# Kernel optimization log

Measured on AMD Instinct MI355X. Metric: run time of the kernel, lower is better.

Reference implementation:

```python
import jax, jax.numpy as jnp
import numpy as np
from jax import lax

HEADS = 8
AGENT = 49            # agent_num
POOL = 7              # int(sqrt(agent_num))
DOWN_H, DOWN_W = 7, 7  # downstream_agent_shape
DIM = 256
WIN = 56              # sqrt(num_patches)


def _resize(x, oh, ow):
    # torch F.interpolate(mode='bilinear', align_corners=False) equivalent for upsample/identity
    return jax.image.resize(x, x.shape[:-2] + (oh, ow), method='bilinear', antialias=False)


def _bias_pipeline(bias, H, W):
    # bias: (heads, AGENT, h0, w0) -> (heads, H*W, DOWN_H*DOWN_W)
    h = bias.shape[0]
    pb = _resize(bias, H, W)                                     # (h, 49, H, W)
    pb = pb.reshape(h, POOL, POOL, H * W).transpose(0, 3, 1, 2)  # (h, HW, 7, 7)
    pb = _resize(pb, DOWN_H, DOWN_W)                             # (h, HW, 7, 7)
    return pb.reshape(h, H * W, DOWN_H * DOWN_W)


def setup_inputs() -> dict:
    key = jax.random.key(0)
    ks = jax.random.split(key, 16)
    b, H, W = 16, WIN, WIN
    n, c, h = H * W, DIM, HEADS
    s = 0.02
    f32 = jnp.float32
    return {
        "x": jax.random.normal(ks[0], (b, n, c), f32),
        "H": H,
        "W": W,
        "Wq": jax.random.normal(ks[1], (c, c), f32) * c ** -0.5,
        "Wkv": jax.random.normal(ks[2], (2 * c, c), f32) * c ** -0.5,
        "Wproj": jax.random.normal(ks[3], (c, c), f32) * c ** -0.5,
        "bproj": jnp.zeros((c,), f32),
        "dwc_w": jax.random.normal(ks[4], (c, 1, 3, 3), f32) * 0.1,
        "dwc_b": jnp.zeros((c,), f32),
        "an_bias": jax.random.normal(ks[5], (h, AGENT, 7, 7), f32) * s,
        "na_bias": jax.random.normal(ks[6], (h, AGENT, 7, 7), f32) * s,
        "ah_bias": jax.random.normal(ks[7], (1, h, AGENT, WIN, 1), f32) * s,
        "aw_bias": jax.random.normal(ks[8], (1, h, AGENT, 1, WIN), f32) * s,
        "ha_bias": jax.random.normal(ks[9], (1, h, WIN, 1, AGENT), f32) * s,
        "wa_bias": jax.random.normal(ks[10], (1, h, 1, WIN, AGENT), f32) * s,
    }


def reference(x, H, W, Wq, Wkv, Wproj, bproj, dwc_w, dwc_b,
              an_bias, na_bias, ah_bias, aw_bias, ha_bias, wa_bias):
    b, n, c = x.shape
    h = HEADS
    hd = c // h
    T = n // 2
    scale = hd ** -0.5
    dan = DOWN_H * DOWN_W

    q_lin = x @ Wq.T                       # (b,n,c)
    kv = x @ Wkv.T                         # (b,n,2c)
    k_lin, v_lin = kv[..., :c], kv[..., c:]

    # adaptive avg pool of q to (7,7) agent grid (H, W divisible by 7)
    qg = q_lin.reshape(b, DOWN_H, H // DOWN_H, DOWN_W, W // DOWN_W, c).mean(axis=(2, 4))
    agent = qg.reshape(b, dan, h, hd).transpose(0, 2, 1, 3)   # (b,h,49,hd)

    q = q_lin.reshape(b, n, h, hd).transpose(0, 2, 1, 3)      # (b,h,n,hd)
    k = k_lin.reshape(b, n, h, hd).transpose(0, 2, 1, 3)
    v = v_lin.reshape(b, n, h, hd).transpose(0, 2, 1, 3)

    # agent -> kv attention biases
    pb1 = _bias_pipeline(an_bias, H, W).transpose(0, 2, 1)    # (h,49,HW)
    pb2 = _bias_pipeline((ah_bias + aw_bias)[0], H, W).transpose(0, 2, 1)
    position_bias = (pb1 + pb2)[None]                         # (1,h,49,HW)

    agent_attn = jax.nn.softmax(
        jnp.einsum('bhad,bhnd->bhan', agent * scale, k) + position_bias, axis=-1)
    agent_v = jnp.einsum('bhan,bhnd->bhad', agent_attn, v)    # (b,h,49,hd)

    # query -> agent attention biases
    ab1 = _bias_pipeline(na_bias, H, W)                       # (h,HW,49)
    ab2 = _bias_pipeline((ha_bias + wa_bias)[0].transpose(0, 3, 1, 2), H, W)
    agent_bias = (ab1 + ab2)[None]                            # (1,h,HW,49)

    # top-T query selection, then bilinear upsample of scores back to n rows
    token_w = jax.nn.softmax(q.mean(axis=-1), axis=-1)        # (b,h,n)
    _, top_idx = lax.top_k(token_w, T)                        # (b,h,T)
    q_top = jnp.take_along_axis(q, top_idx[..., None], axis=2)  # (b,h,T,hd)
    q2 = jnp.einsum('bhtd,bhad->bhta', q_top, agent)          # (b,h,T,49)
    q2 = _resize(q2, n, dan) * scale                          # (b,h,n,49)

    q_attn = jax.nn.softmax(q2 + agent_bias, axis=-1)
    out = jnp.einsum('bhna,bhad->bhnd', q_attn, agent_v)
    out = out.transpose(0, 2, 1, 3).reshape(b, n, c)

    # depthwise conv branch on v
    v_img = v.transpose(0, 2, 1, 3).reshape(b, H, W, c).transpose(0, 3, 1, 2)  # (b,c,H,W)
    dw = lax.conv_general_dilated(v_img, dwc_w, (1, 1), ((1, 1), (1, 1)),
                                  feature_group_count=c)
    dw = dw + dwc_b[None, :, None, None]
    out = out + dw.transpose(0, 2, 3, 1).reshape(b, n, c)
    return out @ Wproj.T + bproj
```

## Files before the change

### kernel.cpp

```cpp
#include <hip/hip_runtime.h>
#include <stdint.h>

typedef _Float16 f16;
typedef _Float16 half8 __attribute__((ext_vector_type(8)));
typedef float f32x4 __attribute__((ext_vector_type(4)));

#define NBATCH 16
#define NTOK 3136
#define NTOT 50176
#define NH 8
#define NA 49
#define NAP 64
#define TTOP 1568
#define SCALE 0.17677669529663687f
#define FPARTS 4

__device__ __forceinline__ f32x4 mfma16(half8 a, half8 b, f32x4 c) {
  return __builtin_amdgcn_mfma_f32_16x16x32_f16(a, b, c, 0, 0, 0);
}

__device__ __forceinline__ void gload16(const void* g, void* l) {
  __builtin_amdgcn_global_load_lds(
      (const __attribute__((address_space(1))) void*)g,
      (__attribute__((address_space(3))) void*)l, 16, 0, 0);
}

__global__ __launch_bounds__(256) void k_prep_w(const float* Wq, const float* Wkv, const float* Wproj,
                                                f16* wqkv, f16* wproj) {
  int total1 = 768 * 256;
  int total = total1 + 256 * 256;
  for (int i = blockIdx.x * 256 + threadIdx.x; i < total; i += gridDim.x * 256) {
    if (i < total1) {
      int j = i >> 8, k = i & 255;
      float v = (j < 256) ? Wq[j * 256 + k] : Wkv[(j - 256) * 256 + k];
      wqkv[i] = (f16)v;
    } else {
      int i2 = i - total1;
      wproj[i2] = (f16)Wproj[i2];
    }
  }
}

__global__ __launch_bounds__(256) void k_cvt_x(const float* x, f16* xh, long total) {
  long i = (long)blockIdx.x * blockDim.x + threadIdx.x;
  long stride = (long)gridDim.x * blockDim.x;
  for (long e = i * 8; e < total; e += stride * 8) {
    float4 v0 = *(const float4*)(x + e);
    float4 v1 = *(const float4*)(x + e + 4);
    half8 o = {(f16)v0.x, (f16)v0.y, (f16)v0.z, (f16)v0.w,
               (f16)v1.x, (f16)v1.y, (f16)v1.z, (f16)v1.w};
    *(half8*)(xh + e) = o;
  }
}

__global__ __launch_bounds__(256) void k_bias(const float* an_b, const float* na_b,
                                              const float* ah_b, const float* aw_b,
                                              const float* ha_b, const float* wa_b,
                                              float* pos_bias, float* agent_bias) {
  int n = blockIdx.x * 256 + threadIdx.x;
  int h = blockIdx.y;
  if (n >= NTOK) return;
  int y = n / 56, x = n - y * 56;
  float py = (y + 0.5f) * 0.125f - 0.5f;
  float px = (x + 0.5f) * 0.125f - 0.5f;
  int iy0 = (int)floorf(py); float fy = py - (float)iy0;
  int ix0 = (int)floorf(px); float fx = px - (float)ix0;
  int y0 = max(iy0, 0), y1 = min(iy0 + 1, 6);
  int x0 = max(ix0, 0), x1 = min(ix0 + 1, 6);
  float w00 = (1.f - fy) * (1.f - fx), w01 = (1.f - fy) * fx;
  float w10 = fy * (1.f - fx), w11 = fy * fx;
  for (int a = 0; a < NA; ++a) {
    const float* pa = an_b + (h * NA + a) * 49;
    float up_an = w00 * pa[y0 * 7 + x0] + w01 * pa[y0 * 7 + x1] +
                  w10 * pa[y1 * 7 + x0] + w11 * pa[y1 * 7 + x1];
    const float* pn = na_b + (h * NA + a) * 49;
    float up_na = w00 * pn[y0 * 7 + x0] + w01 * pn[y0 * 7 + x1] +
                  w10 * pn[y1 * 7 + x0] + w11 * pn[y1 * 7 + x1];
    float pb = up_an + ah_b[(h * NA + a) * 56 + y] + aw_b[(h * NA + a) * 56 + x];
    pos_bias[((size_t)(h * NAP + a)) * NTOK + n] = pb;
    float ab = up_na + ha_b[(h * 56 + y) * NA + a] + wa_b[(h * 56 + x) * NA + a];
    agent_bias[((size_t)(h * NAP + a)) * NTOK + n] = ab;
  }
  for (int a = NA; a < NAP; ++a)
    pos_bias[((size_t)(h * NAP + a)) * NTOK + n] = 0.f;
}

template <bool PROJ>
__global__ __launch_bounds__(256) void k_gemm(const f16* __restrict__ A, const f16* __restrict__ Bw,
                                              f16* __restrict__ CH, float* __restrict__ Cf32,
                                              const float* __restrict__ bias, int N) {
  __shared__ __align__(16) char lds[16384];
  int per = gridDim.x >> 3;
  int wrk = (blockIdx.x & 7) * per + (blockIdx.x >> 3);
  int nNT = N >> 7;
  int mt = wrk / nNT, nt = wrk - mt * nNT;
  int m0 = mt * 128, n0 = nt * 128;
  int tid = threadIdx.x, w = tid >> 6, l = tid & 63, lr = l & 15, lg = l >> 4;
  int wm = w >> 1, wn = w & 1;
  f32x4 acc[4][4] = {};
  const char* Bb = (const char*)Bw + (size_t)n0 * 512;
  int rowA0 = 32 * w + (l >> 2);
  int rowA1 = rowA0 + 16;
  int koff = (l & 3) * 16;
  char* ldsA0 = lds + (2 * w) * 1024;
  char* ldsA1 = lds + (2 * w + 1) * 1024;
  char* ldsB0 = lds + 8192 + (2 * w) * 1024;
  char* ldsB1 = lds + 8192 + (2 * w + 1) * 1024;

  for (int k0 = 0; k0 < 256; k0 += 32) {
    if (PROJ) {
      const char* Ab = (const char*)A + ((size_t)(k0 >> 5) * NTOT + m0) * 64;
      gload16(Ab + (size_t)rowA0 * 64 + koff, ldsA0);
      gload16(Ab + (size_t)rowA1 * 64 + koff, ldsA1);
    } else {
      const char* Ab = (const char*)A + (size_t)m0 * 512 + k0 * 2;
      gload16(Ab + (size_t)rowA0 * 512 + koff, ldsA0);
      gload16(Ab + (size_t)rowA1 * 512 + koff, ldsA1);
    }
    gload16(Bb + (size_t)rowA0 * 512 + k0 * 2 + koff, ldsB0);
    gload16(Bb + (size_t)rowA1 * 512 + k0 * 2 + koff, ldsB1);
    __syncthreads();
    half8 af[4], bf[4];
#pragma unroll
    for (int m4 = 0; m4 < 4; ++m4) {
      int row = wm * 64 + m4 * 16 + lr;
      af[m4] = *(const half8*)(lds + row * 64 + lg * 16);
    }
#pragma unroll
    for (int n4 = 0; n4 < 4; ++n4) {
      int row = wn * 64 + n4 * 16 + lr;
      bf[n4] = *(const half8*)(lds + 8192 + row * 64 + lg * 16);
    }
#pragma unroll
    for (int m4 = 0; m4 < 4; ++m4)
#pragma unroll
      for (int n4 = 0; n4 < 4; ++n4)
        acc[m4][n4] = mfma16(af[m4], bf[n4], acc[m4][n4]);
    __syncthreads();
  }

  if (PROJ) {
#pragma unroll
    for (int n4 = 0; n4 < 4; ++n4) {
      int n = n0 + wn * 64 + n4 * 16 + lr;
#pragma unroll
      for (int m4 = 0; m4 < 4; ++m4)
#pragma unroll
        for (int r = 0; r < 4; ++r) {
          int m = m0 + wm * 64 + m4 * 16 + lg * 4 + r;
          Cf32[(size_t)m * N + n] = acc[m4][n4][r] + bias[n];
        }
    }
  } else {
    f16* cl = (f16*)lds;
    int rr = tid >> 2, c4 = tid & 3;
#pragma unroll
    for (int hm = 0; hm < 2; ++hm) {
      __syncthreads();
      if (wm == hm) {
#pragma unroll
        for (int m4 = 0; m4 < 4; ++m4)
#pragma unroll
          for (int n4 = 0; n4 < 4; ++n4)
#pragma unroll
            for (int r = 0; r < 4; ++r)
              cl[(m4 * 16 + lg * 4 + r) * 128 + wn * 64 + n4 * 16 + lr] = (f16)acc[m4][n4][r];
      }
      __syncthreads();
#pragma unroll
      for (int cc = 0; cc < 4; ++cc) {
        int pn = (n0 >> 5) + cc;
        half8 v = *(const half8*)(cl + rr * 128 + cc * 32 + c4 * 8);
        *(half8*)(CH + ((size_t)pn * NTOT + m0 + hm * 64 + rr) * 32 + c4 * 8) = v;
      }
    }
  }
}

__global__ __launch_bounds__(256) void k_pool_tw(const f16* qkvH, f16* agent, float* tw) {
  int bh = blockIdx.x, b = bh >> 3, h = bh & 7;
  int tid = threadIdx.x;
  const f16* qp0 = qkvH + ((size_t)h * NTOT + (size_t)b * NTOK) * 32;
  {
    int a = tid >> 2, c = tid & 3;
    float s8[8] = {};
    if (a < NA) {
      int dh = a / 7, dwi = a - dh * 7;
      for (int i = 0; i < 8; ++i)
#pragma unroll
        for (int j = 0; j < 8; ++j) {
          int tok = (dh * 8 + i) * 56 + dwi * 8 + j;
          half8 v = *(const half8*)(qp0 + (size_t)tok * 32 + c * 8);
#pragma unroll
          for (int e = 0; e < 8; ++e) s8[e] += (float)v[e];
        }
    }
    half8 o;
#pragma unroll
    for (int e = 0; e < 8; ++e) o[e] = (f16)(s8[e] * (SCALE / 64.f));
    *(half8*)(agent + (size_t)bh * NAP * 32 + a * 32 + c * 8) = o;
  }
  for (int n = tid; n < NTOK; n += 256) {
    const half8* qp = (const half8*)(qp0 + (size_t)n * 32);
    float sum = 0.f;
#pragma unroll
    for (int j = 0; j < 4; ++j) {
      half8 v = qp[j];
#pragma unroll
      for (int e = 0; e < 8; ++e) sum += (float)v[e];
    }
    tw[(size_t)bh * NTOK + n] = sum * (1.f / 32.f);
  }
}

template <int NE, int J>
__device__ __forceinline__ void stage_local(unsigned long long (&key)[NE], int kmask, int base) {
#pragma unroll
  for (int e = 0; e < NE; ++e) {
    if ((e & J) == 0) {
      bool desc = (((base + e) & kmask) == 0);
      unsigned long long a = key[e], c = key[e | J];
      if ((a < c) == desc) { key[e] = c; key[e | J] = a; }
    }
  }
}

__global__ __launch_bounds__(256, 1) void k_sort1(const float* tw, unsigned long long* keys64) {
  __shared__ unsigned long long lk[2048 + 128];
  int bh = blockIdx.x >> 1, half = blockIdx.x & 1;
  int tid = threadIdx.x;
  const float* p = tw + (size_t)bh * NTOK;
  int gbase = half * 2048 + tid * 8;
  unsigned long long key[8];
#pragma unroll
  for (int e = 0; e < 8; ++e) {
    int s = gbase + e;
    float v = (s < NTOK) ? p[s] : -1e30f;
    unsigned ub = __float_as_uint(v);
    ub = (ub & 0x80000000u) ? ~ub : (ub | 0x80000000u);
    unsigned low = (s < NTOK) ? ~(unsigned)s : 0u;
    key[e] = ((unsigned long long)ub << 32) | low;
  }
  stage_local<8, 1>(key, 2, gbase);
  stage_local<8, 2>(key, 4, gbase); stage_local<8, 1>(key, 4, gbase);
  stage_local<8, 4>(key, 8, gbase); stage_local<8, 2>(key, 8, gbase); stage_local<8, 1>(key, 8, gbase);
  for (int k = 16; k <= 2048; k <<= 1) {
    bool desc = ((gbase & k) == 0);
    for (int j = k >> 1; j >= 8; j >>= 1) {
      int m = j >> 3;
      bool takeMax = (((tid & m) == 0) == desc);
      unsigned long long pv[8];
      if (m <= 32) {
#pragma unroll
        for (int e = 0; e < 8; ++e) pv[e] = __shfl_xor(key[e], m, 64);
      } else {
        __syncthreads();
#pragma unroll
        for (int e = 0; e < 8; ++e) { int ix = tid * 8 + e; lk[ix + (ix >> 4)] = key[e]; }
        __syncthreads();
        int pb = (tid ^ m) * 8;
#pragma unroll
        for (int e = 0; e < 8; ++e) { int ix = pb + e; pv[e] = lk[ix + (ix >> 4)]; }
      }
#pragma unroll
      for (int e = 0; e < 8; ++e)
        key[e] = takeMax ? (key[e] > pv[e] ? key[e] : pv[e])
                         : (key[e] < pv[e] ? key[e] : pv[e]);
    }
    stage_local<8, 4>(key, k, gbase);
    stage_local<8, 2>(key, k, gbase);
    stage_local<8, 1>(key, k, gbase);
  }
  unsigned long long* op = keys64 + (size_t)bh * 4096 + gbase;
#pragma unroll
  for (int e = 0; e < 8; ++e) op[e] = key[e];
}

__global__ __launch_bounds__(256, 1) void k_sort2(const unsigned long long* keys64, int* topidx) {
  __shared__ unsigned long long lk[4096 + 256];
  int bh = blockIdx.x, tid = threadIdx.x;
  const unsigned long long* ip = keys64 + (size_t)bh * 4096 + (size_t)tid * 16;
  unsigned long long key[16];
#pragma unroll
  for (int e = 0; e < 16; ++e) key[e] = ip[e];
  int base = tid * 16;
  for (int j = 2048; j >= 16; j >>= 1) {
    int m = j >> 4;
    bool takeMax = ((tid & m) == 0);
    unsigned long long pv[16];
    if (m <= 32) {
#pragma unroll
      for (int e = 0; e < 16; ++e) pv[e] = __shfl_xor(key[e], m, 64);
    } else {
      __syncthreads();
#pragma unroll
      for (int e = 0; e < 16; ++e) { int ix = base + e; lk[ix + (ix >> 4)] = key[e]; }
      __syncthreads();
      int pb = (tid ^ m) * 16;
#pragma unroll
      for (int e = 0; e < 16; ++e) { int ix = pb + e; pv[e] = lk[ix + (ix >> 4)]; }
    }
#pragma unroll
    for (int e = 0; e < 16; ++e)
      key[e] = takeMax ? (key[e] > pv[e] ? key[e] : pv[e])
                       : (key[e] < pv[e] ? key[e] : pv[e]);
  }
  stage_local<16, 8>(key, 4096, base);
  stage_local<16, 4>(key, 4096, base);
  stage_local<16, 2>(key, 4096, base);
  stage_local<16, 1>(key, 4096, base);
  if (tid < TTOP / 16) {
    int* op = topidx + (size_t)bh * TTOP + base;
#pragma unroll
    for (int e = 0; e < 16; ++e) op[e] = (int)(~(unsigned)key[e]);
  }
}

__global__ __launch_bounds__(256) void k_vt(const f16* qkvH, f16* vt) {
  __shared__ __align__(16) f16 t[64][40];
  int bh = blockIdx.y, b = bh >> 3, h = bh & 7;
  int n0 = blockIdx.x * 64;
  int tid = threadIdx.x;
  const f16* vp = qkvH + ((size_t)(16 + h) * NTOT + (size_t)b * NTOK + n0) * 32;
  {
    int nl = tid >> 2, c = tid & 3;
    *(half8*)(&t[nl][c * 8]) = *(const half8*)(vp + (size_t)nl * 32 + c * 8);
  }
  __syncthreads();
  for (int s = tid; s < 64 * 32; s += 256) {
    int d = s >> 6, nl = s & 63;
    vt[((size_t)(bh * 32 + d)) * NTOK + n0 + nl] = t[nl][d];
  }
}

__global__ __launch_bounds__(256) void k_flash(const f16* qkvH, const f16* agent, const f16* vt,
                                               const float* pos_bias, float* opart, float* rspart) {
  __shared__ __align__(16) f16 pbuf[4][64][40];
  __shared__ float ored[64][33];
  __shared__ float rssum[64];
  int part = blockIdx.x, bh = blockIdx.y, b = bh >> 3, h = bh & 7;
  int tid = threadIdx.x, w = tid >> 6, l = tid & 63, lr = l & 15, lg = l >> 4;
  half8 afrag[4];
#pragma unroll
  for (int mt = 0; mt < 4; ++mt)
    afrag[mt] = *(const half8*)(agent + ((size_t)bh * 64 + mt * 16 + lr) * 32 + lg * 8);
  f32x4 o[4][2] = {};
  float rs[4][4] = {};
  const f16* kbase = qkvH + ((size_t)(8 + h) * NTOT + (size_t)b * NTOK) * 32;
  const f16* vtb = vt + (size_t)bh * 32 * NTOK;
  const float* pbb = pos_bias + (size_t)h * NAP * NTOK;
  f32x4 zero = {};
  for (int n0 = (part * 4 + w) * 32; n0 < NTOK; n0 += 512) {
#pragma unroll
    for (int t2 = 0; t2 < 2; ++t2) {
      int nc = n0 + t2 * 16;
      half8 kf = *(const half8*)(kbase + (size_t)(nc + lr) * 32 + lg * 8);
#pragma unroll
      for (int mt = 0; mt < 4; ++mt) {
        f32x4 s = mfma16(afrag[mt], kf, zero);
#pragma unroll
        for (int r = 0; r < 4; ++r) {
          int a = mt * 16 + lg * 4 + r;
          float pv = __expf(s[r] + pbb[(size_t)a * NTOK + nc + lr]);
          rs[mt][r] += pv;
          pbuf[w][a][t2 * 16 + lr] = (f16)pv;
        }
      }
    }
    half8 pf[4];
#pragma unroll
    for (int mt = 0; mt < 4; ++mt)
      pf[mt] = *(const half8*)(&pbuf[w][mt * 16 + lr][lg * 8]);
#pragma unroll
    for (int dt = 0; dt < 2; ++dt) {
      half8 vf = *(const half8*)(vtb + (size_t)(dt * 16 + lr) * NTOK + n0 + lg * 8);
#pragma unroll
      for (int mt = 0; mt < 4; ++mt)
        o[mt][dt] = mfma16(pf[mt], vf, o[mt][dt]);
    }
  }
#pragma unroll
  for (int mt = 0; mt < 4; ++mt)
#pragma unroll
    for (int r = 0; r < 4; ++r) {
      float v = rs[mt][r];
      for (int off = 1; off < 16; off <<= 1) v += __shfl_xor(v, off, 64);
      rs[mt][r] = v;
    }
  for (int s = tid; s < 64 * 33; s += 256) ((float*)ored)[s] = 0.f;
  if (tid < 64) rssum[tid] = 0.f;
  __syncthreads();
  for (int ww = 0; ww < 4; ++ww) {
    if (w == ww) {
      if (lr == 0)
#pragma unroll
        for (int mt = 0; mt < 4; ++mt)
#pragma unroll
          for (int r = 0; r < 4; ++r) rssum[mt * 16 + lg * 4 + r] += rs[mt][r];
#pragma unroll
      for (int mt = 0; mt < 4; ++mt)
#pragma unroll
        for (int dt = 0; dt < 2; ++dt)
#pragma unroll
          for (int r = 0; r < 4; ++r)
            ored[mt * 16 + lg * 4 + r][dt * 16 + lr] += o[mt][dt][r];
    }
    __syncthreads();
  }
  int pp = bh * FPARTS + part;
  for (int s = tid; s < NA * 32; s += 256) {
    int a = s >> 5, d = s & 31;
    opart[((size_t)pp * 64 + a) * 32 + d] = ored[a][d];
  }
  if (tid < NA) rspart[(size_t)pp * 64 + tid] = rssum[tid];
}

__global__ __launch_bounds__(256) void k_fred(const float* opart, const float* rspart, float* agv) {
  int bh = blockIdx.x, tid = threadIdx.x;
  for (int s = tid; s < NA * 32; s += 256) {
    int a = s >> 5, d = s & 31;
    float o = 0.f, rs = 0.f;
#pragma unroll
    for (int p = 0; p < FPARTS; ++p) {
      int pp = bh * FPARTS + p;
      o += opart[((size_t)pp * 64 + a) * 32 + d];
      rs += rspart[(size_t)pp * 64 + a];
    }
    agv[(size_t)bh * NA * 32 + s] = o / rs;
  }
}

__global__ __launch_bounds__(256) void k_po(const f16* __restrict__ qkvH, const f16* __restrict__ agent,
                                            const int* __restrict__ topidx,
                                            const float* __restrict__ agent_bias,
                                            const float* __restrict__ agent_v,
                                            const float* __restrict__ dwc_w,
                                            const float* __restrict__ dwc_b,
                                            f16* __restrict__ preH) {
  __shared__ __align__(16) char uq[9728];
  __shared__ __align__(16) f16 pbuf[7 * 8 * 16 * 8];
  __shared__ __align__(16) f16 avT[32][72];
  __shared__ __align__(16) f16 wconvh[9][32];
  __shared__ float bconv[32];
  f16 (*q2buf)[76] = (f16(*)[76])uq;
  f16 (*ctile)[40] = (f16(*)[40])uq;
  int chunk = blockIdx.x, bh = blockIdx.y, b = bh >> 3, h = bh & 7;
  int tid = threadIdx.x, w = tid >> 6, l = tid & 63, lr = l & 15, lg = l >> 4;
  const f16* qplane = qkvH + ((size_t)h * NTOT + (size_t)b * NTOK) * 32;
  const f16* vp = qkvH + ((size_t)(16 + h) * NTOT + (size_t)b * NTOK) * 32;
  for (int s = tid; s < 32 * 64; s += 256) {
    int d = s >> 6, a = s & 63;
    avT[d][a] = (a < NA) ? (f16)agent_v[((size_t)bh * NA + a) * 32 + d] : (f16)0.f;
  }
  for (int s = tid; s < 32 * 9; s += 256) {
    int d = s / 9, t = s - d * 9;
    wconvh[t][d] = (f16)dwc_w[(size_t)(h * 32 + d) * 9 + t];
  }
  if (tid < 32) bconv[tid] = dwc_b[h * 32 + tid];
  half8 bfrag[4];
#pragma unroll
  for (int nt = 0; nt < 4; ++nt)
    bfrag[nt] = *(const half8*)(agent + ((size_t)bh * 64 + nt * 16 + lr) * 32 + lg * 8);
  int jbase = chunk * 56 - 4;
  f32x4 zero = {};
  {
    int j = jbase + w * 16 + lr;
    int jc = min(max(j, 0), TTOP - 1);
    int tok = topidx[(size_t)bh * TTOP + jc];
    half8 qf = *(const half8*)(qplane + (size_t)tok * 32 + lg * 8);
#pragma unroll
    for (int nt = 0; nt < 4; ++nt) {
      f32x4 s = mfma16(qf, bfrag[nt], zero);
#pragma unroll
      for (int r = 0; r < 4; ++r)
        q2buf[w * 16 + lg * 4 + r][nt * 16 + lr] = (f16)s[r];
    }
  }
  __syncthreads();
  if (tid < 224) {
    int ltok = tid >> 1, hc = tid & 1;
    int g = chunk * 112 + ltok;
    int hi = g >> 1;
    int jA, jB; float wAq, wBq;
    if (g & 1) { jA = hi; jB = hi + 1; wAq = 0.75f; wBq = 0.25f; }
    else       { jA = hi - 1; jB = hi; wAq = 0.25f; wBq = 0.75f; }
    jA = min(max(jA, 0), TTOP - 1);
    jB = min(max(jB, 0), TTOP - 1);
    int lA = jA - jbase, lB = jB - jbase;
    const float* ab = agent_bias + (size_t)h * NAP * NTOK + g;
    float ssum = 0.f;
    half8 oo[4];
#pragma unroll
    for (int cc = 0; cc < 4; ++cc) {
      int c = hc * 4 + cc;
      half8 a8 = *(const half8*)(&q2buf[lA][c * 8]);
      half8 b8 = *(const half8*)(&q2buf[lB][c * 8]);
#pragma unroll
      for (int e = 0; e < 8; ++e) {
        int a = c * 8 + e;
        float pv = 0.f;
        if (a < NA) {
          float v = wAq * (float)a8[e] + wBq * (float)b8[e] + ab[(size_t)a * NTOK];
          pv = __expf(v);
          ssum += pv;
        }
        oo[cc][e] = (f16)pv;
      }
    }
    ssum += __shfl_xor(ssum, 1, 64);
    f16 invs = (f16)(1.f / ssum);
    half8 iv8 = {invs, invs, invs, invs, invs, invs, invs, invs};
    int lt = ltok >> 4, lrr = ltok & 15;
#pragma unroll
    for (int cc = 0; cc < 4; ++cc) {
      int c = hc * 4 + cc;
      *(half8*)(pbuf + ((size_t)(lt * 8 + c) * 16 + lrr) * 8) = oo[cc] * iv8;
    }
  }
  __syncthreads();
  half8 bf[2][2];
#pragma unroll
  for (int nt = 0; nt < 2; ++nt)
#pragma unroll
    for (int ks = 0; ks < 2; ++ks)
      bf[nt][ks] = *(const half8*)(&avT[0][0] + (size_t)(nt * 16 + lr) * 72 + ks * 32 + lg * 8);
#pragma unroll
  for (int i = 0; i < 2; ++i) {
    int lt = w * 2 + i;
    if (lt >= 7) continue;
    half8 pa0 = *(const half8*)(pbuf + ((size_t)(lt * 8 + lg) * 16 + lr) * 8);
    half8 pa1 = *(const half8*)(pbuf + ((size_t)(lt * 8 + 4 + lg) * 16 + lr) * 8);
    f32x4 acc0 = {}, acc1 = {};
    acc0 = mfma16(pa0, bf[0][0], acc0);
    acc0 = mfma16(pa1, bf[0][1], acc0);
    acc1 = mfma16(pa0, bf[1][0], acc1);
    acc1 = mfma16(pa1, bf[1][1], acc1);
    int ltrow = lt * 16 + lg * 4;
#pragma unroll
    for (int r = 0; r < 4; ++r) {
      ctile[ltrow + r][lr] = (f16)acc0[r];
      ctile[ltrow + r][16 + lr] = (f16)acc1[r];
    }
  }
  __syncthreads();
  if (tid >= 224) return;
  int ltok = tid >> 1, hc = tid & 1;
  int g = chunk * 112 + ltok;
  int ly = ltok / 56, x = ltok - ly * 56;
  int y = chunk * 2 + ly;
  half8 acch[2] = {};
#pragma unroll
  for (int ky = 0; ky < 3; ++ky) {
    int gy = y + ky - 1;
    if (gy < 0 || gy >= 56) continue;
#pragma unroll
    for (int kx = 0; kx < 3; ++kx) {
      int xx = x + kx - 1;
      if (xx < 0 || xx >= 56) continue;
      int t = ky * 3 + kx;
      const f16* vt9 = vp + (size_t)(gy * 56 + xx) * 32 + hc * 16;
#pragma unroll
      for (int c = 0; c < 2; ++c) {
        half8 wv = *(const half8*)(&wconvh[t][hc * 16 + c * 8]);
        half8 vv = *(const half8*)(vt9 + c * 8);
        acch[c] += wv * vv;
      }
    }
  }
  f16* op = preH + ((size_t)h * NTOT + (size_t)b * NTOK + g) * 32 + hc * 16;
#pragma unroll
  for (int c = 0; c < 2; ++c) {
    half8 cv = *(const half8*)(&ctile[ltok][hc * 16 + c * 8]);
    half8 o;
#pragma unroll
    for (int e = 0; e < 8; ++e)
      o[e] = (f16)((float)cv[e] + bconv[hc * 16 + c * 8 + e] + (float)acch[c][e]);
    *(half8*)(op + c * 8) = o;
  }
}

extern "C" void kernel_launch(void* const* d_in, const int* in_sizes, int n_in,
                              void* d_out, int out_size, void* d_ws, size_t ws_size,
                              hipStream_t stream) {
  const float* x     = (const float*)d_in[0];
  const float* Wq    = (const float*)d_in[3];
  const float* Wkv   = (const float*)d_in[4];
  const float* Wproj = (const float*)d_in[5];
  const float* bproj = (const float*)d_in[6];
  const float* dwc_w = (const float*)d_in[7];
  const float* dwc_b = (const float*)d_in[8];
  const float* an_b  = (const float*)d_in[9];
  const float* na_b  = (const float*)d_in[10];
  const float* ah_b  = (const float*)d_in[11];
  const float* aw_b  = (const float*)d_in[12];
  const float* ha_b  = (const float*)d_in[13];
  const float* wa_b  = (const float*)d_in[14];

  char* ws = (char*)d_ws;
  size_t off = 0;
  auto alloc = [&](size_t bytes) {
    void* p = ws + off;
    off = (off + bytes + 255) & ~(size_t)255;
    return p;
  };
  f16* wqkv    = (f16*)alloc((size_t)768 * 256 * 2);
  f16* wproj   = (f16*)alloc((size_t)256 * 256 * 2);
  f16* qkvH    = (f16*)alloc((size_t)24 * NTOT * 32 * 2);
  float* posb  = (float*)alloc((size_t)8 * NAP * NTOK * 4);
  float* agb   = (float*)alloc((size_t)8 * NAP * NTOK * 4);
  f16* agent   = (f16*)alloc((size_t)128 * NAP * 32 * 2);
  float* tw    = (float*)alloc((size_t)128 * NTOK * 4);
  int* topidx  = (int*)alloc((size_t)128 * TTOP * 4);
  unsigned long long* keys64 = (unsigned long long*)alloc((size_t)128 * 4096 * 8);
  f16* vt      = (f16*)alloc((size_t)128 * 32 * NTOK * 2);
  float* agv   = (float*)alloc((size_t)128 * NA * 32 * 4);
  float* opart = (float*)alloc((size_t)128 * FPARTS * 64 * 32 * 4);
  float* rspart= (float*)alloc((size_t)128 * FPARTS * 64 * 4);
  f16* preH    = (f16*)alloc((size_t)8 * NTOT * 32 * 2);
  f16* xh      = (f16*)alloc((size_t)NTOT * 256 * 2);

  k_prep_w<<<1024, 256, 0, stream>>>(Wq, Wkv, Wproj, wqkv, wproj);
  k_cvt_x<<<2048, 256, 0, stream>>>(x, xh, (long)NTOT * 256);
  k_bias<<<dim3(13, 8), 256, 0, stream>>>(an_b, na_b, ah_b, aw_b, ha_b, wa_b, posb, agb);
  k_gemm<false><<<2352, 256, 0, stream>>>(xh, wqkv, qkvH, nullptr, nullptr, 768);
  k_pool_tw<<<128, 256, 0, stream>>>(qkvH, agent, tw);
  k_sort1<<<256, 256, 0, stream>>>(tw, keys64);
  k_sort2<<<128, 256, 0, stream>>>(keys64, topidx);
  k_vt<<<dim3(49, 128), 256, 0, stream>>>(qkvH, vt);
  k_flash<<<dim3(FPARTS, 128), 256, 0, stream>>>(qkvH, agent, vt, posb, opart, rspart);
  k_fred<<<128, 256, 0, stream>>>(opart, rspart, agv);
  k_po<<<dim3(28, 128), 256, 0, stream>>>(qkvH, agent, topidx, agb, agv, dwc_w, dwc_b, preH);
  k_gemm<true><<<784, 256, 0, stream>>>(preH, wproj, nullptr, (float*)d_out, bproj, 256);
}
```

Measured before the change: 226.3 us.

## Stage projection output through LDS, double flash partitions, swizzle pbuf, use packed half blend

The projection GEMM epilogue now stages its fp32 accumulators in LDS by quadrant and writes coalesced float4 rows with the bias added, replacing scattered scalar stores. The flash kernel's split count goes from 4 to 8 partitions to expose more parallelism. The query-interpolation blend is computed in packed fp16, which costs some precision. The pbuf store/load addresses are XOR-swizzled to reduce LDS bank conflicts. The extra syncs in the epilogue and the larger partial-reduction workload are the trade-offs.

```diff
diff --git a/kernel.cpp b/kernel.cpp
--- a/kernel.cpp
+++ b/kernel.cpp
@@ -13,7 +13,7 @@
 #define NAP 64
 #define TTOP 1568
 #define SCALE 0.17677669529663687f
-#define FPARTS 4
+#define FPARTS 8
 
 __device__ __forceinline__ f32x4 mfma16(half8 a, half8 b, f32x4 c) {
   return __builtin_amdgcn_mfma_f32_16x16x32_f16(a, b, c, 0, 0, 0);
@@ -140,17 +140,35 @@
   }
 
   if (PROJ) {
-#pragma unroll
-    for (int n4 = 0; n4 < 4; ++n4) {
-      int n = n0 + wn * 64 + n4 * 16 + lr;
-#pragma unroll
-      for (int m4 = 0; m4 < 4; ++m4)
-#pragma unroll
-        for (int r = 0; r < 4; ++r) {
-          int m = m0 + wm * 64 + m4 * 16 + lg * 4 + r;
-          Cf32[(size_t)m * N + n] = acc[m4][n4][r] + bias[n];
+    float* cl32 = (float*)lds;
+    int rr = tid >> 2, qc = tid & 3;
+#pragma unroll
+    for (int hm = 0; hm < 2; ++hm)
+#pragma unroll
+      for (int hn = 0; hn < 2; ++hn) {
+        __syncthreads();
+        if (wm == hm && wn == hn) {
+#pragma unroll
+          for (int m4 = 0; m4 < 4; ++m4)
+#pragma unroll
+            for (int n4 = 0; n4 < 4; ++n4)
+#pragma unroll
+              for (int r = 0; r < 4; ++r)
+                cl32[(m4 * 16 + lg * 4 + r) * 64 + n4 * 16 + lr] = acc[m4][n4][r];
         }
-    }
+        __syncthreads();
+        int gm = m0 + hm * 64 + rr;
+        int gn = n0 + hn * 64 + qc * 16;
+        const float4* src = (const float4*)(cl32 + rr * 64 + qc * 16);
+        float4* dst = (float4*)(Cf32 + (size_t)gm * N + gn);
+        const float4* bp = (const float4*)(bias + gn);
+#pragma unroll
+        for (int q = 0; q < 4; ++q) {
+          float4 v = src[q], bb = bp[q];
+          v.x += bb.x; v.y += bb.y; v.z += bb.z; v.w += bb.w;
+          dst[q] = v;
+        }
+      }
   } else {
     f16* cl = (f16*)lds;
     int rr = tid >> 2, c4 = tid & 3;
@@ -350,7 +368,7 @@
   const f16* vtb = vt + (size_t)bh * 32 * NTOK;
   const float* pbb = pos_bias + (size_t)h * NAP * NTOK;
   f32x4 zero = {};
-  for (int n0 = (part * 4 + w) * 32; n0 < NTOK; n0 += 512) {
+  for (int n0 = (part * 4 + w) * 32; n0 < NTOK; n0 += 32 * FPARTS * 4) {
 #pragma unroll
     for (int t2 = 0; t2 < 2; ++t2) {
       int nc = n0 + t2 * 16;
@@ -488,6 +506,9 @@
     jB = min(max(jB, 0), TTOP - 1);
     int lA = jA - jbase, lB = jB - jbase;
     const float* ab = agent_bias + (size_t)h * NAP * NTOK + g;
+    f16 wAh = (f16)wAq, wBh = (f16)wBq;
+    half8 wA8 = {wAh, wAh, wAh, wAh, wAh, wAh, wAh, wAh};
+    half8 wB8 = {wBh, wBh, wBh, wBh, wBh, wBh, wBh, wBh};
     float ssum = 0.f;
     half8 oo[4];
 #pragma unroll
@@ -495,12 +516,13 @@
       int c = hc * 4 + cc;
       half8 a8 = *(const half8*)(&q2buf[lA][c * 8]);
       half8 b8 = *(const half8*)(&q2buf[lB][c * 8]);
+      half8 v8 = a8 * wA8 + b8 * wB8;
 #pragma unroll
       for (int e = 0; e < 8; ++e) {
         int a = c * 8 + e;
         float pv = 0.f;
         if (a < NA) {
-          float v = wAq * (float)a8[e] + wBq * (float)b8[e] + ab[(size_t)a * NTOK];
+          float v = (float)v8[e] + ab[(size_t)a * NTOK];
           pv = __expf(v);
           ssum += pv;
         }
@@ -514,7 +536,8 @@
 #pragma unroll
     for (int cc = 0; cc < 4; ++cc) {
       int c = hc * 4 + cc;
-      *(half8*)(pbuf + ((size_t)(lt * 8 + c) * 16 + lrr) * 8) = oo[cc] * iv8;
+      int idx = (((lt * 8 + c) * 16 + lrr) * 8) ^ (hc * 16);
+      *(half8*)(pbuf + idx) = oo[cc] * iv8;
     }
   }
   __syncthreads();
@@ -528,8 +551,8 @@
   for (int i = 0; i < 2; ++i) {
     int lt = w * 2 + i;
     if (lt >= 7) continue;
-    half8 pa0 = *(const half8*)(pbuf + ((size_t)(lt * 8 + lg) * 16 + lr) * 8);
-    half8 pa1 = *(const half8*)(pbuf + ((size_t)(lt * 8 + 4 + lg) * 16 + lr) * 8);
+    half8 pa0 = *(const half8*)(pbuf + (((size_t)(lt * 8 + lg) * 16 + lr) * 8));
+    half8 pa1 = *(const half8*)(pbuf + ((((size_t)(lt * 8 + 4 + lg) * 16 + lr) * 8) ^ 16));
     f32x4 acc0 = {}, acc1 = {};
     acc0 = mfma16(pa0, bf[0][0], acc0);
     acc0 = mfma16(pa1, bf[0][1], acc0);
```

Measured after the change: 251.0 us. 10.9% more time.
